# Optimization experiments

Hardware: AMD Instinct MI355X
Metric: run time of the kernel (lower is better)

The kernel has to match this reference:

```python
import jax, jax.numpy as jnp
import numpy as np

ALPHA = 0.1  # GCN2Conv alpha; theta=None => beta=1.0 so out = ((1-a)*prop + a*x0) @ W


def gcn_norm(edge_index, n):
    # PyG gcn_norm with add_self_loops=True and unit edge weights.
    row, col = edge_index[0], edge_index[1]
    loop = jnp.arange(n, dtype=edge_index.dtype)
    row = jnp.concatenate([row, loop])
    col = jnp.concatenate([col, loop])
    w = jnp.ones(row.shape[0], dtype=jnp.float32)
    deg = jax.ops.segment_sum(w, col, num_segments=n)
    dis = jnp.where(deg > 0, jax.lax.rsqrt(jnp.maximum(deg, 1e-12)), 0.0)
    norm = dis[row] * w * dis[col]
    return row, col, norm


def propagate(x, row, col, norm, n):
    # out[col] += norm * x[row]  (source->target aggregation)
    return jax.ops.segment_sum(x[row] * norm[:, None], col, num_segments=n)


def setup_inputs() -> dict:
    key = jax.random.key(0)
    ks = jax.random.split(key, 6)
    N, E, F, L = 100000, 1000000, 64, 4
    x = jax.random.normal(ks[0], (N, F), dtype=jnp.float32)
    edge_index = jax.random.randint(ks[1], (2, E), 0, N, dtype=jnp.int64)
    gcn2_w = jax.random.normal(ks[2], (L, F, F), dtype=jnp.float32) * (1.0 / np.sqrt(F))
    w1 = jax.random.normal(ks[3], (F, 16), dtype=jnp.float32) * (1.0 / np.sqrt(F))
    b1 = jnp.zeros((16,), dtype=jnp.float32)
    w2 = jax.random.normal(ks[4], (16, 1), dtype=jnp.float32) * (1.0 / np.sqrt(16))
    b2 = jnp.zeros((1,), dtype=jnp.float32)
    return {"x": x, "edge_index": edge_index, "gcn2_w": gcn2_w,
            "w1": w1, "b1": b1, "w2": w2, "b2": b2}


def reference(x, edge_index, gcn2_w, w1, b1, w2, b2):
    n = x.shape[0]
    row, col, norm = gcn_norm(edge_index, n)
    x0 = x
    h = x
    # GCN2Conv stack: h = relu(((1-a)*Ah + a*x0) @ W)
    for l in range(gcn2_w.shape[0]):
        p = propagate(h, row, col, norm, n)
        h = jax.nn.relu(((1.0 - ALPHA) * p + ALPHA * x0) @ gcn2_w[l])
    # GCNConv(F,16): lin -> propagate -> bias
    h = propagate(h @ w1, row, col, norm, n) + b1
    # GCNConv(16,1)
    h = propagate(h @ w2, row, col, norm, n) + b2
    return jax.nn.sigmoid(h).squeeze(1).astype(jnp.float32)
```

## Files before the change

### kernel.cpp

```cpp
#include <hip/hip_runtime.h>
#include <hip/hip_fp16.h>
#include <math.h>

#define ALPHA 0.1f
#define CHUNK 8192
#define CAP 2048

typedef _Float16 f16x8 __attribute__((ext_vector_type(8)));
typedef float f32x4 __attribute__((ext_vector_type(4)));

static __device__ __forceinline__ void nt_store_half(__half* p, float v) {
    __builtin_nontemporal_store((_Float16)v, (_Float16*)p);
}


__global__ void k_init(int* bcur, int nbuck,
                       const float* __restrict__ gw, const float* __restrict__ w1,
                       __half* __restrict__ whT, __half* __restrict__ w1T, int L) {
    int i = blockIdx.x * blockDim.x + threadIdx.x;
    if (i < nbuck) bcur[i] = 0;
    int tot = L * 4096;
    if (i < tot) {
        int l = i >> 12, r = i & 4095;
        int k = r >> 6, nf = r & 63;
        whT[(l << 12) + nf * 64 + k] = __float2half(gw[i]);
    } else if (i < tot + 1024) {
        int r = i - tot;
        int k = r >> 4, nf = r & 15;
        w1T[nf * 64 + k] = __float2half(w1[r]);
    }
}


__global__ __launch_bounds__(256) void kb_part(const int* __restrict__ row,
                                               const int* __restrict__ col,
                                               int e, int nbuck,
                                               int* __restrict__ cursor,
                                               int* __restrict__ part) {
    __shared__ int lcnt[1024];
    __shared__ int lbase[1024];
    int t = threadIdx.x;
    for (int i = t; i < 1024; i += 256) lcnt[i] = 0;
    __syncthreads();
    int base = blockIdx.x * CHUNK;
    int end = min(base + CHUNK, e);
    for (int i = base + t; i < end; i += 256)
        atomicAdd(&lcnt[col[i] >> 7], 1);
    __syncthreads();
    for (int i = t; i < nbuck; i += 256) {
        int c = lcnt[i];
        lbase[i] = c ? atomicAdd(&cursor[i], c) : 0;
    }
    __syncthreads();
    for (int i = t; i < 1024; i += 256) lcnt[i] = 0;
    __syncthreads();
    for (int i = base + t; i < end; i += 256) {
        int cl = col[i];
        int b = cl >> 7;
        int lp = lbase[b] + atomicAdd(&lcnt[b], 1);
        if (lp < CAP) part[b * CAP + lp] = ((cl & 127) << 17) | row[i];
    }
}


__global__ __launch_bounds__(256) void kb_csr(const int* __restrict__ bcur,
                                              const int* __restrict__ part, int n,
                                              const float* __restrict__ x,
                                              float* __restrict__ dis,
                                              int2* __restrict__ off2,
                                              int* __restrict__ srow,
                                              __half* __restrict__ xs,
                                              __half* __restrict__ x0h) {
    __shared__ int cnt[128], excl[128], stmp[128];
    __shared__ float disl[128];
    int b = blockIdx.x;
    int t = threadIdx.x;
    int bstart = b * CAP;
    int bend = bstart + min(bcur[b], CAP);
    if (t < 128) cnt[t] = 0;
    __syncthreads();
    for (int i = bstart + t; i < bend; i += 256)
        atomicAdd(&cnt[part[i] >> 17], 1);
    __syncthreads();
    if (t < 128) stmp[t] = cnt[t];
    __syncthreads();
    for (int d = 1; d < 128; d <<= 1) {
        int add = (t < 128 && t >= d) ? stmp[t - d] : 0;
        __syncthreads();
        if (t < 128) stmp[t] += add;
        __syncthreads();
    }
    if (t < 128) {
        excl[t] = stmp[t] - cnt[t];
        int c = (b << 7) + t;
        float d = rsqrtf((float)cnt[t] + 1.0f);
        disl[t] = d;
        if (c < n) {
            off2[c] = make_int2(bstart + stmp[t] - cnt[t], bstart + stmp[t]);
            dis[c] = d;
        }
        cnt[t] = 0;
    }
    __syncthreads();
    for (int i = bstart + t; i < bend; i += 256) {
        int pk = part[i];
        int cl = pk >> 17;
        int lp = atomicAdd(&cnt[cl], 1);
        srow[bstart + excl[cl] + lp] = pk & 0x1FFFF;
    }
    int c0 = b << 7;
    for (int i = t; i < 128 * 64; i += 256) {
        int node = c0 + (i >> 6);
        if (node >= n) break;
        float xv = x[(size_t)node * 64 + (i & 63)];
        float d = disl[i >> 6];
        xs[(size_t)node * 64 + (i & 63)] = __float2half(d * xv);
        x0h[(size_t)node * 64 + (i & 63)] = __float2half(ALPHA * xv);
    }
}


__global__ __launch_bounds__(256) void k_gcn2_fused(
    const int* __restrict__ srow, const int2* __restrict__ off2,
    const float* __restrict__ dis, const __half* __restrict__ hs_in,
    const __half* __restrict__ x0h, const __half* __restrict__ whT,
    __half* __restrict__ hs_out,
    const __half* __restrict__ w1T,
    __half* __restrict__ t16s, int n)
{
    __shared__ __half vs[32][72];
    __shared__ __half vs2[32][72];
    __shared__ float dcs[32];

    int t = threadIdx.x;
    int w = t >> 6;
    int lane = t & 63;
    int nb = blockIdx.x * 32;
    int m16 = lane & 15;
    int quad = lane >> 4;

    f16x8 bf0 = *(const f16x8*)(whT + (size_t)(w * 16 + m16) * 64 + quad * 8);
    f16x8 bf1 = *(const f16x8*)(whT + (size_t)(w * 16 + m16) * 64 + 32 + quad * 8);

    int j = lane >> 3;
    int s = lane & 7;
    int local = w * 8 + j;
    int c = nb + local;
    bool valid = c < n;
    int cc = valid ? c : 0;
    int2 se = off2[cc];
    int start = se.x;
    int end = valid ? se.y : se.x;
    float dc = dis[cc];

    float a0, a1, a2, a3, a4, a5, a6, a7;
    float b0 = 0, b1 = 0, b2 = 0, b3 = 0, b4 = 0, b5 = 0, b6 = 0, b7 = 0;
    {
        f16x8 q = *(const f16x8*)(hs_in + (size_t)cc * 64 + s * 8);
        a0 = (float)q[0]; a1 = (float)q[1]; a2 = (float)q[2]; a3 = (float)q[3];
        a4 = (float)q[4]; a5 = (float)q[5]; a6 = (float)q[6]; a7 = (float)q[7];
    }
    int e = start;
    for (; e + 2 <= end; e += 2) {
        int r0 = srow[e];
        int r1 = srow[e + 1];
        f16x8 q0 = *(const f16x8*)(hs_in + (size_t)r0 * 64 + s * 8);
        f16x8 q1 = *(const f16x8*)(hs_in + (size_t)r1 * 64 + s * 8);
        a0 += (float)q0[0]; a1 += (float)q0[1]; a2 += (float)q0[2]; a3 += (float)q0[3];
        a4 += (float)q0[4]; a5 += (float)q0[5]; a6 += (float)q0[6]; a7 += (float)q0[7];
        b0 += (float)q1[0]; b1 += (float)q1[1]; b2 += (float)q1[2]; b3 += (float)q1[3];
        b4 += (float)q1[4]; b5 += (float)q1[5]; b6 += (float)q1[6]; b7 += (float)q1[7];
    }
    if (e < end) {
        int r0 = srow[e];
        f16x8 q0 = *(const f16x8*)(hs_in + (size_t)r0 * 64 + s * 8);
        a0 += (float)q0[0]; a1 += (float)q0[1]; a2 += (float)q0[2]; a3 += (float)q0[3];
        a4 += (float)q0[4]; a5 += (float)q0[5]; a6 += (float)q0[6]; a7 += (float)q0[7];
    }
    a0 += b0; a1 += b1; a2 += b2; a3 += b3;
    a4 += b4; a5 += b5; a6 += b6; a7 += b7;

    if (valid) {
        float dc9 = (1.0f - ALPHA) * dc;
        const f16x8* xp = (const f16x8*)(x0h + (size_t)cc * 64 + s * 8);
        f16x8 xv = __builtin_nontemporal_load(xp);
        f16x8 vv;
        vv[0] = (_Float16)(dc9 * a0 + (float)xv[0]);
        vv[1] = (_Float16)(dc9 * a1 + (float)xv[1]);
        vv[2] = (_Float16)(dc9 * a2 + (float)xv[2]);
        vv[3] = (_Float16)(dc9 * a3 + (float)xv[3]);
        vv[4] = (_Float16)(dc9 * a4 + (float)xv[4]);
        vv[5] = (_Float16)(dc9 * a5 + (float)xv[5]);
        vv[6] = (_Float16)(dc9 * a6 + (float)xv[6]);
        vv[7] = (_Float16)(dc9 * a7 + (float)xv[7]);
        *(f16x8*)&vs[local][s * 8] = vv;
        if (s == 0) dcs[local] = dc;
    }
    __syncthreads();

    bool last = (w1T != nullptr);
#pragma unroll
    for (int mt = 0; mt < 2; mt++) {
        f32x4 acc = {0.0f, 0.0f, 0.0f, 0.0f};
        f16x8 af0 = *(const f16x8*)&vs[mt * 16 + m16][quad * 8];
        f16x8 af1 = *(const f16x8*)&vs[mt * 16 + m16][32 + quad * 8];
        acc = __builtin_amdgcn_mfma_f32_16x16x32_f16(af0, bf0, acc, 0, 0, 0);
        acc = __builtin_amdgcn_mfma_f32_16x16x32_f16(af1, bf1, acc, 0, 0, 0);
        if (!last) {
#pragma unroll
            for (int r = 0; r < 4; r++) {
                int loc = mt * 16 + quad * 4 + r;
                int cn = nb + loc;
                if (cn < n) {
                    float h = fmaxf(acc[r], 0.0f);
                    nt_store_half(hs_out + (size_t)cn * 64 + w * 16 + m16, dcs[loc] * h);
                }
            }
        } else {
#pragma unroll
            for (int r = 0; r < 4; r++) {
                int loc = mt * 16 + quad * 4 + r;
                vs2[loc][w * 16 + m16] = __float2half(fmaxf(acc[r], 0.0f));
            }
        }
    }

    if (last) {
        __syncthreads();
        if (w < 2) {
            f16x8 w10 = *(const f16x8*)(w1T + (size_t)m16 * 64 + quad * 8);
            f16x8 w11 = *(const f16x8*)(w1T + (size_t)m16 * 64 + 32 + quad * 8);
            f16x8 af0 = *(const f16x8*)&vs2[w * 16 + m16][quad * 8];
            f16x8 af1 = *(const f16x8*)&vs2[w * 16 + m16][32 + quad * 8];
            f32x4 acc = {0.0f, 0.0f, 0.0f, 0.0f};
            acc = __builtin_amdgcn_mfma_f32_16x16x32_f16(af0, w10, acc, 0, 0, 0);
            acc = __builtin_amdgcn_mfma_f32_16x16x32_f16(af1, w11, acc, 0, 0, 0);
#pragma unroll
            for (int r = 0; r < 4; r++) {
                int loc = w * 16 + quad * 4 + r;
                int cn = nb + loc;
                if (cn < n)
                    nt_store_half(t16s + (size_t)cn * 16 + m16, dcs[loc] * acc[r]);
            }
        }
    }
}


__global__ __launch_bounds__(256) void k_prop16_lin2(
    const int* __restrict__ srow, const int2* __restrict__ off2,
    const float* __restrict__ dis, const __half* __restrict__ t16s,
    const float* __restrict__ b1, const float* __restrict__ w2,
    float* __restrict__ t1s, int n)
{
    int t = threadIdx.x;
    int w = t >> 6, lane = t & 63;
    int g = lane >> 2;
    int s = lane & 3;
    int c = blockIdx.x * 4 + w;
    if (c >= n) return;
    int2 se = off2[c];
    int start = se.x, end = se.y;
    float a0 = 0, a1 = 0, a2 = 0, a3 = 0;
    if (g == 0) {
        float2 q = *(const float2*)(t16s + (size_t)c * 16 + s * 4);
        float2 u;
        u = __half22float2(*(__half2*)&q.x); a0 = u.x; a1 = u.y;
        u = __half22float2(*(__half2*)&q.y); a2 = u.x; a3 = u.y;
    }
    for (int e = start + g; e < end; e += 16) {
        int r = srow[e];
        float2 q = *(const float2*)(t16s + (size_t)r * 16 + s * 4);
        float2 u;
        u = __half22float2(*(__half2*)&q.x); a0 += u.x; a1 += u.y;
        u = __half22float2(*(__half2*)&q.y); a2 += u.x; a3 += u.y;
    }
#pragma unroll
    for (int d = 4; d <= 32; d <<= 1) {
        a0 += __shfl_xor(a0, d, 64); a1 += __shfl_xor(a1, d, 64);
        a2 += __shfl_xor(a2, d, 64); a3 += __shfl_xor(a3, d, 64);
    }
    float dc = dis[c];
    float4 b = *(const float4*)(b1 + s * 4);
    float4 ww = *(const float4*)(w2 + s * 4);
    float partial = (dc * a0 + b.x) * ww.x + (dc * a1 + b.y) * ww.y +
                    (dc * a2 + b.z) * ww.z + (dc * a3 + b.w) * ww.w;
    partial += __shfl_xor(partial, 1, 64);
    partial += __shfl_xor(partial, 2, 64);
    if (lane == 0) t1s[c] = dc * partial;
}


__global__ void k_prop1(const int* __restrict__ srow, const int2* __restrict__ off2,
                        const float* __restrict__ dis, const float* __restrict__ t1s,
                        const float* __restrict__ b2, float* __restrict__ out, int n) {
    int c = blockIdx.x * blockDim.x + threadIdx.x;
    if (c >= n) return;
    int2 se = off2[c];
    float ssum = t1s[c];
    for (int e = se.x; e < se.y; e++) ssum += t1s[srow[e]];
    float v = dis[c] * ssum + b2[0];
    out[c] = 1.0f / (1.0f + expf(-v));
}


static inline char* align16(char* p) {
    return (char*)(((uintptr_t)p + 15) & ~(uintptr_t)15);
}

extern "C" void kernel_launch(void* const* d_in, const int* in_sizes, int n_in,
                              void* d_out, int out_size, void* d_ws, size_t ws_size,
                              hipStream_t stream) {
    const float* x  = (const float*)d_in[0];
    const int*   ei = (const int*)d_in[1];
    const float* gw = (const float*)d_in[2];
    const float* w1 = (const float*)d_in[3];
    const float* b1 = (const float*)d_in[4];
    const float* w2 = (const float*)d_in[5];
    const float* b2 = (const float*)d_in[6];
    float* out = (float*)d_out;

    const int N = in_sizes[0] / 64;
    const int E = in_sizes[1] / 2;
    const int L = in_sizes[2] / (64 * 64);

    const int* row = ei;
    const int* col = ei + E;

    const int NB = (N + 127) >> 7;

    char* p = (char*)d_ws;
    int2* off2 = (int2*)p;         p = align16(p + (size_t)N * 8);
    float* dis = (float*)p;        p = align16(p + (size_t)N * 4);
    int* srow = (int*)p;           p = align16(p + (size_t)NB * CAP * 4);
    int* bcur = (int*)p;           p = align16(p + (size_t)NB * 4);
    __half* whT = (__half*)p;      p = align16(p + (size_t)L * 4096 * 2);
    __half* w1T = (__half*)p;      p = align16(p + 1024 * 2);
    __half* hsA = (__half*)p;      p = align16(p + (size_t)N * 128);
    __half* hsB = (__half*)p;      p = align16(p + (size_t)N * 128);
    __half* x0h = (__half*)p;      p = align16(p + (size_t)N * 128);
    __half* t16s = (__half*)p;     p = align16(p + (size_t)N * 32);
    float* t1s = (float*)p;
    int* part = (int*)hsB;

    const int B = 256;
    int gN = (N + B - 1) / B;
    int gPart = (E + CHUNK - 1) / CHUNK;
    int gInit = (L * 4096 + 1024 + B - 1) / B;
    if (gInit < (NB + B - 1) / B) gInit = (NB + B - 1) / B;

    k_init<<<gInit, B, 0, stream>>>(bcur, NB, gw, w1, whT, w1T, L);
    kb_part<<<gPart, B, 0, stream>>>(row, col, E, NB, bcur, part);
    kb_csr<<<NB, B, 0, stream>>>(bcur, part, N, x, dis, off2, srow, hsA, x0h);

    __half* bufs[2] = {hsA, hsB};
    const __half* hin = hsA;
    for (int l = 0; l < L; l++) {
        bool lastl = (l == L - 1);
        __half* hout = lastl ? nullptr : bufs[(l + 1) & 1];
        k_gcn2_fused<<<(N + 31) / 32, B, 0, stream>>>(
            srow, off2, dis, hin, x0h, whT + (size_t)l * 4096,
            hout, lastl ? w1T : nullptr, t16s, N);
        hin = hout;
    }

    k_prop16_lin2<<<(N + 3) / 4, B, 0, stream>>>(srow, off2, dis, t16s, b1, w2, t1s, N);
    k_prop1<<<gN, B, 0, stream>>>(srow, off2, dis, t1s, b2, out, N);
}
```

Measured before the change: 326.7 us.

## Fold w1·w2 before propagation to reduce 16-wide gather to scalar

Uses linearity to precompute w1@w2 and b1@w2, so the last GCN2 layer outputs one scalar per node instead of a 16-wide feature vector. The 16-channel propagation kernel becomes a scalar per-node gather like the final one, cutting gather bandwidth about 16x for that stage and dropping an MFMA. The trade-off is a different floating-point summation order and a thread-per-node gather loop that may have more load imbalance.

```diff
diff --git a/kernel.cpp b/kernel.cpp
--- a/kernel.cpp
+++ b/kernel.cpp
@@ -16,7 +16,9 @@
 
 __global__ void k_init(int* bcur, int nbuck,
                        const float* __restrict__ gw, const float* __restrict__ w1,
-                       __half* __restrict__ whT, __half* __restrict__ w1T, int L) {
+                       const float* __restrict__ b1, const float* __restrict__ w2,
+                       __half* __restrict__ whT, float* __restrict__ w1w2,
+                       float* __restrict__ betap, int L) {
     int i = blockIdx.x * blockDim.x + threadIdx.x;
     if (i < nbuck) bcur[i] = 0;
     int tot = L * 4096;
@@ -24,10 +26,17 @@
         int l = i >> 12, r = i & 4095;
         int k = r >> 6, nf = r & 63;
         whT[(l << 12) + nf * 64 + k] = __float2half(gw[i]);
-    } else if (i < tot + 1024) {
-        int r = i - tot;
-        int k = r >> 4, nf = r & 15;
-        w1T[nf * 64 + k] = __float2half(w1[r]);
+    } else if (i < tot + 64) {
+        int k = i - tot;
+        float s = 0.0f;
+#pragma unroll
+        for (int j = 0; j < 16; j++) s += w1[k * 16 + j] * w2[j];
+        w1w2[k] = s;
+    } else if (i == tot + 64) {
+        float s = 0.0f;
+#pragma unroll
+        for (int j = 0; j < 16; j++) s += b1[j] * w2[j];
+        *betap = s;
     }
 }
 
@@ -125,8 +134,8 @@
     const float* __restrict__ dis, const __half* __restrict__ hs_in,
     const __half* __restrict__ x0h, const __half* __restrict__ whT,
     __half* __restrict__ hs_out,
-    const __half* __restrict__ w1T,
-    __half* __restrict__ t16s, int n)
+    const float* __restrict__ w1w2,
+    float* __restrict__ us, int n)
 {
     __shared__ __half vs[32][72];
     __shared__ __half vs2[32][72];
@@ -198,7 +207,7 @@
     }
     __syncthreads();
 
-    bool last = (w1T != nullptr);
+    bool last = (w1w2 != nullptr);
 #pragma unroll
     for (int mt = 0; mt < 2; mt++) {
         f32x4 acc = {0.0f, 0.0f, 0.0f, 0.0f};
@@ -227,79 +236,47 @@
 
     if (last) {
         __syncthreads();
-        if (w < 2) {
-            f16x8 w10 = *(const f16x8*)(w1T + (size_t)m16 * 64 + quad * 8);
-            f16x8 w11 = *(const f16x8*)(w1T + (size_t)m16 * 64 + 32 + quad * 8);
-            f16x8 af0 = *(const f16x8*)&vs2[w * 16 + m16][quad * 8];
-            f16x8 af1 = *(const f16x8*)&vs2[w * 16 + m16][32 + quad * 8];
-            f32x4 acc = {0.0f, 0.0f, 0.0f, 0.0f};
-            acc = __builtin_amdgcn_mfma_f32_16x16x32_f16(af0, w10, acc, 0, 0, 0);
-            acc = __builtin_amdgcn_mfma_f32_16x16x32_f16(af1, w11, acc, 0, 0, 0);
-#pragma unroll
-            for (int r = 0; r < 4; r++) {
-                int loc = w * 16 + quad * 4 + r;
-                int cn = nb + loc;
-                if (cn < n)
-                    nt_store_half(t16s + (size_t)cn * 16 + m16, dcs[loc] * acc[r]);
-            }
-        }
-    }
-}
-
-
-__global__ __launch_bounds__(256) void k_prop16_lin2(
-    const int* __restrict__ srow, const int2* __restrict__ off2,
-    const float* __restrict__ dis, const __half* __restrict__ t16s,
-    const float* __restrict__ b1, const float* __restrict__ w2,
-    float* __restrict__ t1s, int n)
-{
-    int t = threadIdx.x;
-    int w = t >> 6, lane = t & 63;
-    int g = lane >> 2;
-    int s = lane & 3;
-    int c = blockIdx.x * 4 + w;
+        int loc = t >> 3;
+        int oct = t & 7;
+        f16x8 hv = *(const f16x8*)&vs2[loc][oct * 8];
+        const float* wp = w1w2 + oct * 8;
+        float u = (float)hv[0] * wp[0] + (float)hv[1] * wp[1] +
+                  (float)hv[2] * wp[2] + (float)hv[3] * wp[3] +
+                  (float)hv[4] * wp[4] + (float)hv[5] * wp[5] +
+                  (float)hv[6] * wp[6] + (float)hv[7] * wp[7];
+        u += __shfl_xor(u, 1, 64);
+        u += __shfl_xor(u, 2, 64);
+        u += __shfl_xor(u, 4, 64);
+        int cn = nb + loc;
+        if (oct == 0 && cn < n)
+            us[cn] = dcs[loc] * u;
+    }
+}
+
+
+__global__ void k_propA(const int* __restrict__ srow, const int2* __restrict__ off2,
+                        const float* __restrict__ dis, const float* __restrict__ us,
+                        const float* __restrict__ betap, float* __restrict__ zs, int n) {
+    int c = blockIdx.x * blockDim.x + threadIdx.x;
     if (c >= n) return;
     int2 se = off2[c];
-    int start = se.x, end = se.y;
-    float a0 = 0, a1 = 0, a2 = 0, a3 = 0;
-    if (g == 0) {
-        float2 q = *(const float2*)(t16s + (size_t)c * 16 + s * 4);
-        float2 u;
-        u = __half22float2(*(__half2*)&q.x); a0 = u.x; a1 = u.y;
-        u = __half22float2(*(__half2*)&q.y); a2 = u.x; a3 = u.y;
-    }
-    for (int e = start + g; e < end; e += 16) {
-        int r = srow[e];
-        float2 q = *(const float2*)(t16s + (size_t)r * 16 + s * 4);
-        float2 u;
-        u = __half22float2(*(__half2*)&q.x); a0 += u.x; a1 += u.y;
-        u = __half22float2(*(__half2*)&q.y); a2 += u.x; a3 += u.y;
-    }
-#pragma unroll
-    for (int d = 4; d <= 32; d <<= 1) {
-        a0 += __shfl_xor(a0, d, 64); a1 += __shfl_xor(a1, d, 64);
-        a2 += __shfl_xor(a2, d, 64); a3 += __shfl_xor(a3, d, 64);
-    }
+    float s = us[c];
+    for (int e = se.x; e < se.y; e++) s += us[srow[e]];
     float dc = dis[c];
-    float4 b = *(const float4*)(b1 + s * 4);
-    float4 ww = *(const float4*)(w2 + s * 4);
-    float partial = (dc * a0 + b.x) * ww.x + (dc * a1 + b.y) * ww.y +
-                    (dc * a2 + b.z) * ww.z + (dc * a3 + b.w) * ww.w;
-    partial += __shfl_xor(partial, 1, 64);
-    partial += __shfl_xor(partial, 2, 64);
-    if (lane == 0) t1s[c] = dc * partial;
-}
-
-
-__global__ void k_prop1(const int* __restrict__ srow, const int2* __restrict__ off2,
-                        const float* __restrict__ dis, const float* __restrict__ t1s,
+    float z = dc * s + *betap;
+    zs[c] = dc * z;
+}
+
+
+__global__ void k_propB(const int* __restrict__ srow, const int2* __restrict__ off2,
+                        const float* __restrict__ dis, const float* __restrict__ zs,
                         const float* __restrict__ b2, float* __restrict__ out, int n) {
     int c = blockIdx.x * blockDim.x + threadIdx.x;
     if (c >= n) return;
     int2 se = off2[c];
-    float ssum = t1s[c];
-    for (int e = se.x; e < se.y; e++) ssum += t1s[srow[e]];
-    float v = dis[c] * ssum + b2[0];
+    float s = zs[c];
+    for (int e = se.x; e < se.y; e++) s += zs[srow[e]];
+    float v = dis[c] * s + b2[0];
     out[c] = 1.0f / (1.0f + expf(-v));
 }
 
@@ -335,21 +312,22 @@
     int* srow = (int*)p;           p = align16(p + (size_t)NB * CAP * 4);
     int* bcur = (int*)p;           p = align16(p + (size_t)NB * 4);
     __half* whT = (__half*)p;      p = align16(p + (size_t)L * 4096 * 2);
-    __half* w1T = (__half*)p;      p = align16(p + 1024 * 2);
+    float* w1w2 = (float*)p;       p = align16(p + 64 * 4);
+    float* betap = (float*)p;      p = align16(p + 16);
     __half* hsA = (__half*)p;      p = align16(p + (size_t)N * 128);
     __half* hsB = (__half*)p;      p = align16(p + (size_t)N * 128);
     __half* x0h = (__half*)p;      p = align16(p + (size_t)N * 128);
-    __half* t16s = (__half*)p;     p = align16(p + (size_t)N * 32);
-    float* t1s = (float*)p;
+    float* us = (float*)p;         p = align16(p + (size_t)N * 4);
+    float* zs = (float*)p;
     int* part = (int*)hsB;
 
     const int B = 256;
     int gN = (N + B - 1) / B;
     int gPart = (E + CHUNK - 1) / CHUNK;
-    int gInit = (L * 4096 + 1024 + B - 1) / B;
+    int gInit = (L * 4096 + 65 + B - 1) / B;
     if (gInit < (NB + B - 1) / B) gInit = (NB + B - 1) / B;
 
-    k_init<<<gInit, B, 0, stream>>>(bcur, NB, gw, w1, whT, w1T, L);
+    k_init<<<gInit, B, 0, stream>>>(bcur, NB, gw, w1, b1, w2, whT, w1w2, betap, L);
     kb_part<<<gPart, B, 0, stream>>>(row, col, E, NB, bcur, part);
     kb_csr<<<NB, B, 0, stream>>>(bcur, part, N, x, dis, off2, srow, hsA, x0h);
 
@@ -360,10 +338,10 @@
         __half* hout = lastl ? nullptr : bufs[(l + 1) & 1];
         k_gcn2_fused<<<(N + 31) / 32, B, 0, stream>>>(
             srow, off2, dis, hin, x0h, whT + (size_t)l * 4096,
-            hout, lastl ? w1T : nullptr, t16s, N);
+            hout, lastl ? w1w2 : nullptr, us, N);
         hin = hout;
     }
 
-    k_prop16_lin2<<<(N + 3) / 4, B, 0, stream>>>(srow, off2, dis, t16s, b1, w2, t1s, N);
-    k_prop1<<<gN, B, 0, stream>>>(srow, off2, dis, t1s, b2, out, N);
-}
+    k_propA<<<gN, B, 0, stream>>>(srow, off2, dis, us, betap, zs, N);
+    k_propB<<<gN, B, 0, stream>>>(srow, off2, dis, zs, b2, out, N);
+}
```

Measured after the change: 307.2 us. 6.0% less time.
